# Kernel optimization log

Hardware: AMD Instinct MI355X
Metric: run time of the kernel (lower is better)

The kernel has to match this reference:

```python
import jax, jax.numpy as jnp
import numpy as np

N = 10000   # function nodes
E = 160000  # edges (avg in/out degree ~16)
C = 8       # hidden channels per function node (fix_hidden_channels=True)
B = 64      # batch
EPS = 1e-5


def setup_inputs() -> dict:
    key = jax.random.key(0)
    ks = jax.random.split(key, 6)
    x = jax.random.normal(ks[0], (B, E), jnp.float32)
    # xavier-ish scale for fan_in ~ avg_degree=16
    w1 = jax.random.normal(ks[1], (E, C), jnp.float32) * 0.25
    b1 = jnp.zeros((N, C), jnp.float32)
    w3 = jax.random.normal(ks[2], (E, C), jnp.float32) * 0.25
    b3 = jnp.zeros((E,), jnp.float32)
    gamma = jnp.ones((N, C), jnp.float32)
    beta = jnp.zeros((N, C), jnp.float32)
    edge_src = jax.random.randint(ks[3], (E,), 0, N, dtype=jnp.int32)
    edge_dst = jax.random.randint(ks[4], (E,), 0, N, dtype=jnp.int32)
    return dict(x=x, w1=w1, b1=b1, gamma=gamma, beta=beta, w3=w3, b3=b3,
                edge_src=edge_src, edge_dst=edge_dst)


def reference(x, w1, b1, gamma, beta, w3, b3, edge_src, edge_dst):
    # --- lin1: SparseLinear (E -> N*C); W1[e, (v,k)] != 0 iff v == dst(e) ---
    # out1[b, v, k] = sum_{e: dst(e)==v} x[b, e] * w1[e, k] + b1[v, k]
    vals = x.T[:, :, None] * w1[:, None, :]                    # [E, B, C]
    h = jax.ops.segment_sum(vals, edge_dst, num_segments=N)    # [N, B, C]
    h = jnp.transpose(h, (1, 0, 2)) + b1                       # [B, N, C]
    # --- GroupLayerNorm: normalize over each node's C-channel group ---
    mu = jnp.mean(h, axis=-1, keepdims=True)
    var = jnp.var(h, axis=-1, keepdims=True)
    h = (h - mu) * jax.lax.rsqrt(var + EPS) * gamma + beta
    # --- nonlin (ELU); dropout p=0 in eval mode -> identity ---
    h = jax.nn.elu(h)
    # --- lin3: SparseLinear (N*C -> E); W3[(v,k), e] != 0 iff v == src(e) ---
    # out[b, e] = sum_k h[b, src(e), k] * w3[e, k] + b3[e]
    g = h[:, edge_src, :]                                      # [B, E, C]
    out = jnp.einsum('bec,ec->be', g, w3) + b3                 # [B, E]
    # --- residual ---
    return out + x
```

## Files before the change

kernel.cpp:

```cpp
#include <hip/hip_runtime.h>

#define N_NODES 10000
#define N_EDGES 160000
#define NC 8
#define LN_EPS 1e-5f

typedef _Float16 h4_t __attribute__((ext_vector_type(4)));
typedef _Float16 h8_t __attribute__((ext_vector_type(8)));

__device__ __forceinline__ int swz(int e, int b) {
  return e * 64 + ((((b >> 2) ^ ((e >> 2) & 15)) << 2) | (b & 3));
}

__global__ void hist_kernel(const int* __restrict__ edst, int* __restrict__ cnt_dst) {
  const int e = blockIdx.x * 256 + threadIdx.x;
  if (e < N_EDGES) atomicAdd(&cnt_dst[edst[e]], 1);
}

__global__ void __launch_bounds__(1024) scan_kernel(
    const int* __restrict__ cnt, int* __restrict__ start, int* __restrict__ cur) {
  const int t = threadIdx.x;
  const int lane = t & 63;
  const int wid = t >> 6;
  const int lo = t * 10;
  const int hi = min(lo + 10, N_NODES);
  int s = 0;
  for (int i = lo; i < hi; ++i) s += cnt[i];
  const int own = s;
#pragma unroll
  for (int d = 1; d < 64; d <<= 1) {
    const int v = __shfl_up(s, d, 64);
    if (lane >= d) s += v;
  }
  __shared__ int wsum[16];
  if (lane == 63) wsum[wid] = s;
  __syncthreads();
  if (t == 0) {
    int acc = 0;
#pragma unroll
    for (int i = 0; i < 16; ++i) { acc += wsum[i]; wsum[i] = acc; }
  }
  __syncthreads();
  int base = (wid ? wsum[wid - 1] : 0) + s - own;
  for (int i = lo; i < hi; ++i) {
    start[i] = base;
    cur[i] = base;
    base += cnt[i];
  }
  if (t == 1023) start[N_NODES] = base;
}

__global__ void __launch_bounds__(256) prep_kernel(
    const float* __restrict__ x, const int* __restrict__ edst,
    int* __restrict__ cur_dst, _Float16* __restrict__ xT_d,
    int* __restrict__ sorted_dst) {
  __shared__ float tile[64 * 64];
  __shared__ int pP[64];
  const int e0 = blockIdx.x * 64;
  const int t = threadIdx.x;

  if (t < 64) {
    const int e = e0 + t;
    const int p = atomicAdd(&cur_dst[edst[e]], 1);
    pP[t] = p;
    sorted_dst[p] = e;
  }

  const int u = t & 15;
  const int row = t >> 4;
#pragma unroll
  for (int j = 0; j < 4; ++j) {
    const int b = j * 16 + row;
    const float4 xv = *(const float4*)&x[(size_t)b * N_EDGES + e0 + 4 * u];
    tile[swz(4 * u + 0, b)] = xv.x;
    tile[swz(4 * u + 1, b)] = xv.y;
    tile[swz(4 * u + 2, b)] = xv.z;
    tile[swz(4 * u + 3, b)] = xv.w;
  }
  __syncthreads();
#pragma unroll
  for (int j = 0; j < 4; ++j) {
    const int r = j * 16 + row;
    const float4 vv = *(const float4*)&tile[r * 64 + ((u ^ ((r >> 2) & 15)) << 2)];
    h4_t hv;
    hv[0] = (_Float16)vv.x; hv[1] = (_Float16)vv.y;
    hv[2] = (_Float16)vv.z; hv[3] = (_Float16)vv.w;
    *(h4_t*)&xT_d[(size_t)pP[r] * 64 + 4 * u] = hv;
  }
}

__global__ void __launch_bounds__(256) node_kernel(
    const _Float16* __restrict__ xT_d, const int* __restrict__ sorted_dst,
    const float* __restrict__ w1, const float* __restrict__ b1,
    const float* __restrict__ gamma, const float* __restrict__ beta,
    const int* __restrict__ start_dst, _Float16* __restrict__ v) {
  const int n = blockIdx.x * 4 + (threadIdx.x >> 6);
  const int b = threadIdx.x & 63;

  float a[NC];
#pragma unroll
  for (int c = 0; c < NC; ++c) a[c] = 0.f;

  const int s0 = start_dst[n];
  const int s1 = start_dst[n + 1];
  int i = s0;
  for (; i + 4 <= s1; i += 4) {
    int ee[4];
#pragma unroll
    for (int k = 0; k < 4; ++k) ee[k] = sorted_dst[i + k];
    float xe[4];
#pragma unroll
    for (int k = 0; k < 4; ++k) xe[k] = (float)xT_d[(size_t)(i + k) * 64 + b];
    float4 wla[4], wlb[4];
#pragma unroll
    for (int k = 0; k < 4; ++k) {
      const float4* wp = (const float4*)(w1 + (size_t)ee[k] * NC);
      wla[k] = wp[0]; wlb[k] = wp[1];
    }
#pragma unroll
    for (int k = 0; k < 4; ++k) {
      a[0] += xe[k] * wla[k].x; a[1] += xe[k] * wla[k].y;
      a[2] += xe[k] * wla[k].z; a[3] += xe[k] * wla[k].w;
      a[4] += xe[k] * wlb[k].x; a[5] += xe[k] * wlb[k].y;
      a[6] += xe[k] * wlb[k].z; a[7] += xe[k] * wlb[k].w;
    }
  }
  for (; i < s1; ++i) {
    const int e = sorted_dst[i];
    const float xe = (float)xT_d[(size_t)i * 64 + b];
    const float4* wp = (const float4*)(w1 + (size_t)e * NC);
    const float4 wa = wp[0], wb = wp[1];
    a[0] += xe * wa.x; a[1] += xe * wa.y; a[2] += xe * wa.z; a[3] += xe * wa.w;
    a[4] += xe * wb.x; a[5] += xe * wb.y; a[6] += xe * wb.z; a[7] += xe * wb.w;
  }

  const float4* b1p = (const float4*)(b1 + (size_t)n * NC);
  const float4 b1a = b1p[0], b1b = b1p[1];
  a[0] += b1a.x; a[1] += b1a.y; a[2] += b1a.z; a[3] += b1a.w;
  a[4] += b1b.x; a[5] += b1b.y; a[6] += b1b.z; a[7] += b1b.w;

  float mu = 0.f;
#pragma unroll
  for (int c = 0; c < NC; ++c) mu += a[c];
  mu *= 0.125f;
  float var = 0.f;
#pragma unroll
  for (int c = 0; c < NC; ++c) { a[c] -= mu; var += a[c] * a[c]; }
  var *= 0.125f;
  const float rs = rsqrtf(var + LN_EPS);

  const float4* gp = (const float4*)(gamma + (size_t)n * NC);
  const float4 ga = gp[0], gb = gp[1];
  const float4* bp = (const float4*)(beta + (size_t)n * NC);
  const float4 ba = bp[0], bb = bp[1];
  float w[NC];
  w[0] = a[0] * rs * ga.x + ba.x;  w[1] = a[1] * rs * ga.y + ba.y;
  w[2] = a[2] * rs * ga.z + ba.z;  w[3] = a[3] * rs * ga.w + ba.w;
  w[4] = a[4] * rs * gb.x + bb.x;  w[5] = a[5] * rs * gb.y + bb.y;
  w[6] = a[6] * rs * gb.z + bb.z;  w[7] = a[7] * rs * gb.w + bb.w;
#pragma unroll
  for (int c = 0; c < NC; ++c) w[c] = w[c] > 0.f ? w[c] : expm1f(w[c]);

  h8_t hv;
#pragma unroll
  for (int c = 0; c < NC; ++c) hv[c] = (_Float16)w[c];
  *(h8_t*)&v[(size_t)n * 512 + b * NC] = hv;
}

__global__ void __launch_bounds__(256) edge_kernel(
    const _Float16* __restrict__ v, const float* __restrict__ w3,
    const float* __restrict__ b3, const float* __restrict__ x,
    const int* __restrict__ esrc, float* __restrict__ out) {
  __shared__ float tile[64 * 64];
  const int e0 = blockIdx.x * 64;
  const int t = threadIdx.x;
  const int w = t >> 6;
  const int b = t & 63;

  int sidx = 0;
  if (b < 16) sidx = esrc[e0 + w * 16 + b];

#pragma unroll 8
  for (int r = 0; r < 16; ++r) {
    const int s = __shfl(sidx, r, 64);
    const h8_t hv = *(const h8_t*)&v[(size_t)s * 512 + b * NC];
    const float4* wp = (const float4*)(w3 + (size_t)(e0 + w * 16 + r) * NC);
    const float4 wa = wp[0], wb = wp[1];
    const float dot =
        (float)hv[0] * wa.x + (float)hv[1] * wa.y + (float)hv[2] * wa.z + (float)hv[3] * wa.w +
        (float)hv[4] * wb.x + (float)hv[5] * wb.y + (float)hv[6] * wb.z + (float)hv[7] * wb.w;
    tile[swz(w * 16 + r, b)] = dot;
  }
  __syncthreads();

  const int u = t & 15;
  const int row = t >> 4;
  const float4 bb = *(const float4*)&b3[e0 + 4 * u];
#pragma unroll
  for (int j = 0; j < 4; ++j) {
    const int bo = j * 16 + row;
    const float o0 = tile[swz(4 * u + 0, bo)];
    const float o1 = tile[swz(4 * u + 1, bo)];
    const float o2 = tile[swz(4 * u + 2, bo)];
    const float o3 = tile[swz(4 * u + 3, bo)];
    const float4 xb = *(const float4*)&x[(size_t)bo * N_EDGES + e0 + 4 * u];
    float4 o;
    o.x = o0 + bb.x + xb.x;  o.y = o1 + bb.y + xb.y;
    o.z = o2 + bb.z + xb.z;  o.w = o3 + bb.w + xb.w;
    *(float4*)&out[(size_t)bo * N_EDGES + e0 + 4 * u] = o;
  }
}

extern "C" void kernel_launch(void* const* d_in, const int* in_sizes, int n_in,
                              void* d_out, int out_size, void* d_ws, size_t ws_size,
                              hipStream_t stream) {
  const float* x     = (const float*)d_in[0];
  const float* w1    = (const float*)d_in[1];
  const float* b1    = (const float*)d_in[2];
  const float* gamma = (const float*)d_in[3];
  const float* beta  = (const float*)d_in[4];
  const float* w3    = (const float*)d_in[5];
  const float* b3    = (const float*)d_in[6];
  const int* esrc    = (const int*)d_in[7];
  const int* edst    = (const int*)d_in[8];
  float* out = (float*)d_out;

  char* ws = (char*)d_ws;
  size_t off = 0;
  auto alloc = [&](size_t bytes) -> void* {
    void* p = ws + off;
    off += (bytes + 255) & ~(size_t)255;
    return p;
  };
  _Float16* xT_d   = (_Float16*)alloc((size_t)N_EDGES * 64 * 2);
  _Float16* v      = (_Float16*)alloc((size_t)N_NODES * 512 * 2);
  int* sorted_dst  = (int*)alloc((size_t)N_EDGES * 4);
  int* cnt_dst     = (int*)alloc((size_t)N_NODES * 4);
  int* start_dst   = (int*)alloc((size_t)(N_NODES + 1) * 4);
  int* cur_dst     = (int*)alloc((size_t)N_NODES * 4);

  hipMemsetAsync(cnt_dst, 0, (size_t)N_NODES * 4, stream);

  hist_kernel<<<N_EDGES / 256, 256, 0, stream>>>(edst, cnt_dst);
  scan_kernel<<<1, 1024, 0, stream>>>(cnt_dst, start_dst, cur_dst);
  prep_kernel<<<N_EDGES / 64, 256, 0, stream>>>(x, edst, cur_dst, xT_d, sorted_dst);
  node_kernel<<<N_NODES / 4, 256, 0, stream>>>(xT_d, sorted_dst, w1, b1, gamma, beta,
                                               start_dst, v);
  edge_kernel<<<N_EDGES / 64, 256, 0, stream>>>(v, w3, b3, x, esrc, out);
}
```

Before: 193.7 us.

## Fuse lin3 into node kernel via source-sorted CSR and add finalize transpose pass

```diff
diff --git a/kernel.cpp b/kernel.cpp
--- a/kernel.cpp
+++ b/kernel.cpp
@@ -12,13 +12,23 @@
   return e * 64 + ((((b >> 2) ^ ((e >> 2) & 15)) << 2) | (b & 3));
 }
 
-__global__ void hist_kernel(const int* __restrict__ edst, int* __restrict__ cnt_dst) {
+__global__ void hist_kernel(const int* __restrict__ edst, const int* __restrict__ esrc,
+                            int* __restrict__ cnt_dst, int* __restrict__ cnt_src) {
   const int e = blockIdx.x * 256 + threadIdx.x;
-  if (e < N_EDGES) atomicAdd(&cnt_dst[edst[e]], 1);
+  if (e < N_EDGES) {
+    atomicAdd(&cnt_dst[edst[e]], 1);
+    atomicAdd(&cnt_src[esrc[e]], 1);
+  }
 }
 
 __global__ void __launch_bounds__(1024) scan_kernel(
-    const int* __restrict__ cnt, int* __restrict__ start, int* __restrict__ cur) {
+    const int* __restrict__ cnt_dst, const int* __restrict__ cnt_src,
+    int* __restrict__ start_dst, int* __restrict__ cur_dst,
+    int* __restrict__ start_src, int* __restrict__ cur_src) {
+  const int* cnt = blockIdx.x ? cnt_src : cnt_dst;
+  int* start = blockIdx.x ? start_src : start_dst;
+  int* cur   = blockIdx.x ? cur_src   : cur_dst;
+
   const int t = threadIdx.x;
   const int lane = t & 63;
   const int wid = t >> 6;
@@ -52,8 +62,9 @@
 
 __global__ void __launch_bounds__(256) prep_kernel(
     const float* __restrict__ x, const int* __restrict__ edst,
-    int* __restrict__ cur_dst, _Float16* __restrict__ xT_d,
-    int* __restrict__ sorted_dst) {
+    const int* __restrict__ esrc, int* __restrict__ cur_dst,
+    int* __restrict__ cur_src, _Float16* __restrict__ xT_d,
+    int* __restrict__ sorted_dst, int* __restrict__ sorted_src) {
   __shared__ float tile[64 * 64];
   __shared__ int pP[64];
   const int e0 = blockIdx.x * 64;
@@ -64,6 +75,8 @@
     const int p = atomicAdd(&cur_dst[edst[e]], 1);
     pP[t] = p;
     sorted_dst[p] = e;
+    const int q = atomicAdd(&cur_src[esrc[e]], 1);
+    sorted_src[q] = e;
   }
 
   const int u = t & 15;
@@ -93,7 +106,9 @@
     const _Float16* __restrict__ xT_d, const int* __restrict__ sorted_dst,
     const float* __restrict__ w1, const float* __restrict__ b1,
     const float* __restrict__ gamma, const float* __restrict__ beta,
-    const int* __restrict__ start_dst, _Float16* __restrict__ v) {
+    const int* __restrict__ start_dst,
+    const int* __restrict__ sorted_src, const int* __restrict__ start_src,
+    const float* __restrict__ w3, _Float16* __restrict__ outT) {
   const int n = blockIdx.x * 4 + (threadIdx.x >> 6);
   const int b = threadIdx.x & 63;
 
@@ -161,40 +176,54 @@
 #pragma unroll
   for (int c = 0; c < NC; ++c) w[c] = w[c] > 0.f ? w[c] : expm1f(w[c]);
 
-  h8_t hv;
-#pragma unroll
-  for (int c = 0; c < NC; ++c) hv[c] = (_Float16)w[c];
-  *(h8_t*)&v[(size_t)n * 512 + b * NC] = hv;
-}
-
-__global__ void __launch_bounds__(256) edge_kernel(
-    const _Float16* __restrict__ v, const float* __restrict__ w3,
-    const float* __restrict__ b3, const float* __restrict__ x,
-    const int* __restrict__ esrc, float* __restrict__ out) {
+  const int t0 = start_src[n];
+  const int t1 = start_src[n + 1];
+  int j = t0;
+  for (; j + 4 <= t1; j += 4) {
+    int ee[4];
+#pragma unroll
+    for (int k = 0; k < 4; ++k) ee[k] = sorted_src[j + k];
+    float4 wla[4], wlb[4];
+#pragma unroll
+    for (int k = 0; k < 4; ++k) {
+      const float4* wp = (const float4*)(w3 + (size_t)ee[k] * NC);
+      wla[k] = wp[0]; wlb[k] = wp[1];
+    }
+#pragma unroll
+    for (int k = 0; k < 4; ++k) {
+      const float dot = w[0] * wla[k].x + w[1] * wla[k].y + w[2] * wla[k].z + w[3] * wla[k].w +
+                        w[4] * wlb[k].x + w[5] * wlb[k].y + w[6] * wlb[k].z + w[7] * wlb[k].w;
+      outT[(size_t)ee[k] * 64 + b] = (_Float16)dot;
+    }
+  }
+  for (; j < t1; ++j) {
+    const int e = sorted_src[j];
+    const float4* wp = (const float4*)(w3 + (size_t)e * NC);
+    const float4 wa = wp[0], wb = wp[1];
+    const float dot = w[0] * wa.x + w[1] * wa.y + w[2] * wa.z + w[3] * wa.w +
+                      w[4] * wb.x + w[5] * wb.y + w[6] * wb.z + w[7] * wb.w;
+    outT[(size_t)e * 64 + b] = (_Float16)dot;
+  }
+}
+
+__global__ void __launch_bounds__(256) finalize_kernel(
+    const _Float16* __restrict__ outT, const float* __restrict__ b3,
+    const float* __restrict__ x, float* __restrict__ out) {
   __shared__ float tile[64 * 64];
   const int e0 = blockIdx.x * 64;
   const int t = threadIdx.x;
-  const int w = t >> 6;
-  const int b = t & 63;
-
-  int sidx = 0;
-  if (b < 16) sidx = esrc[e0 + w * 16 + b];
-
-#pragma unroll 8
-  for (int r = 0; r < 16; ++r) {
-    const int s = __shfl(sidx, r, 64);
-    const h8_t hv = *(const h8_t*)&v[(size_t)s * 512 + b * NC];
-    const float4* wp = (const float4*)(w3 + (size_t)(e0 + w * 16 + r) * NC);
-    const float4 wa = wp[0], wb = wp[1];
-    const float dot =
-        (float)hv[0] * wa.x + (float)hv[1] * wa.y + (float)hv[2] * wa.z + (float)hv[3] * wa.w +
-        (float)hv[4] * wb.x + (float)hv[5] * wb.y + (float)hv[6] * wb.z + (float)hv[7] * wb.w;
-    tile[swz(w * 16 + r, b)] = dot;
-  }
-  __syncthreads();
-
   const int u = t & 15;
   const int row = t >> 4;
+#pragma unroll
+  for (int j = 0; j < 4; ++j) {
+    const int e = j * 16 + row;
+    const h4_t hv = *(const h4_t*)&outT[(size_t)(e0 + e) * 64 + 4 * u];
+    float4 fv;
+    fv.x = (float)hv[0]; fv.y = (float)hv[1];
+    fv.z = (float)hv[2]; fv.w = (float)hv[3];
+    *(float4*)&tile[e * 64 + ((u ^ ((e >> 2) & 15)) << 2)] = fv;
+  }
+  __syncthreads();
   const float4 bb = *(const float4*)&b3[e0 + 4 * u];
 #pragma unroll
   for (int j = 0; j < 4; ++j) {
@@ -233,18 +262,25 @@
     return p;
   };
   _Float16* xT_d   = (_Float16*)alloc((size_t)N_EDGES * 64 * 2);
-  _Float16* v      = (_Float16*)alloc((size_t)N_NODES * 512 * 2);
+  _Float16* outT   = (_Float16*)alloc((size_t)N_EDGES * 64 * 2);
   int* sorted_dst  = (int*)alloc((size_t)N_EDGES * 4);
+  int* sorted_src  = (int*)alloc((size_t)N_EDGES * 4);
   int* cnt_dst     = (int*)alloc((size_t)N_NODES * 4);
+  int* cnt_src     = (int*)alloc((size_t)N_NODES * 4);
   int* start_dst   = (int*)alloc((size_t)(N_NODES + 1) * 4);
+  int* start_src   = (int*)alloc((size_t)(N_NODES + 1) * 4);
   int* cur_dst     = (int*)alloc((size_t)N_NODES * 4);
-
-  hipMemsetAsync(cnt_dst, 0, (size_t)N_NODES * 4, stream);
-
-  hist_kernel<<<N_EDGES / 256, 256, 0, stream>>>(edst, cnt_dst);
-  scan_kernel<<<1, 1024, 0, stream>>>(cnt_dst, start_dst, cur_dst);
-  prep_kernel<<<N_EDGES / 64, 256, 0, stream>>>(x, edst, cur_dst, xT_d, sorted_dst);
+  int* cur_src     = (int*)alloc((size_t)N_NODES * 4);
+
+  hipMemsetAsync(cnt_dst, 0, (size_t)2 * N_NODES * 4 + 512, stream);
+
+  hist_kernel<<<N_EDGES / 256, 256, 0, stream>>>(edst, esrc, cnt_dst, cnt_src);
+  scan_kernel<<<2, 1024, 0, stream>>>(cnt_dst, cnt_src, start_dst, cur_dst,
+                                      start_src, cur_src);
+  prep_kernel<<<N_EDGES / 64, 256, 0, stream>>>(x, edst, esrc, cur_dst, cur_src,
+                                                xT_d, sorted_dst, sorted_src);
   node_kernel<<<N_NODES / 4, 256, 0, stream>>>(xT_d, sorted_dst, w1, b1, gamma, beta,
-                                               start_dst, v);
-  edge_kernel<<<N_EDGES / 64, 256, 0, stream>>>(v, w3, b3, x, esrc, out);
-}
+                                               start_dst, sorted_src, start_src,
+                                               w3, outT);
+  finalize_kernel<<<N_EDGES / 64, 256, 0, stream>>>(outT, b3, x, out);
+}
```

Result: slower. 208.7 us (+7.7%).
